# Kernel tuning notes

Measured on AMD Instinct MI355X. Metric: run time of the kernel, lower is better.

The kernel has to match this reference:

```python
import jax, jax.numpy as jnp
import numpy as np
import math

NUM_HEADS = 16


def setup_inputs() -> dict:
    key = jax.random.key(0)
    ks = jax.random.split(key, 5)
    L, B, E = 2048, 2, 1024
    scale = 1.0 / math.sqrt(E)
    return {
        "query": jax.random.normal(ks[0], (L, B, E), jnp.float32),
        "key": jax.random.normal(ks[1], (L, B, E), jnp.float32),
        "value": jax.random.normal(ks[2], (L, B, E), jnp.float32),
        "in_proj_weight": jax.random.normal(ks[3], (3 * E, E), jnp.float32) * scale,
        "in_proj_bias": jnp.zeros((3 * E,), jnp.float32),
        "out_w": jax.random.normal(ks[4], (E, E), jnp.float32) * scale,
        "out_b": jnp.zeros((E,), jnp.float32),
    }


def reference(query, key, value, in_proj_weight, in_proj_bias, out_w, out_b):
    L, Bz, E = query.shape
    S = key.shape[0]
    H = NUM_HEADS
    hd = E // H
    # in-projection: chunk packed weight into q/k/v parts (same math as torch chunk)
    w_q, w_k, w_v = jnp.split(in_proj_weight, 3, axis=0)
    b_q, b_k, b_v = jnp.split(in_proj_bias, 3, axis=0)
    q = query @ w_q.T + b_q            # (L, B, E)
    k = key @ w_k.T + b_k              # (S, B, E)
    v = value @ w_v.T + b_v            # (S, B, E)
    # (L, B*H, hd) -> (B*H, L, hd)
    q = q.reshape(L, Bz * H, hd).transpose(1, 0, 2) / math.sqrt(hd)
    k = k.reshape(S, Bz * H, hd).transpose(1, 0, 2)
    v = v.reshape(S, Bz * H, hd).transpose(1, 0, 2)
    # sigmoid attention (non-softmax), full (B*H, L, S) matrix as in original
    attn = jax.nn.sigmoid(jnp.einsum("bld,bsd->bls", q, k))
    denom = attn.sum(axis=-1, keepdims=True) + 1e-4
    out = jnp.einsum("bls,bsd->bld", attn / denom, v)  # (B*H, L, hd)
    out = out.transpose(1, 0, 2).reshape(L, Bz, E)
    out = out @ out_w.T + out_b
    avg_weights = attn.reshape(Bz, H, L, S).sum(axis=1) / H
    return out, avg_weights
```

## Files before the change

kernel.cpp:

```cpp
#include <hip/hip_runtime.h>
#include <stdint.h>


#define L_SEQ 2048
#define NBATCH 2
#define EMB 1024
#define NHEAD 16
#define HD 64
#define MROWS 4096

typedef __bf16 bf16x8 __attribute__((ext_vector_type(8)));
typedef float f32x4 __attribute__((ext_vector_type(4)));

#define WAITVM(N) asm volatile("s_waitcnt vmcnt(" #N ")" ::: "memory")
#define WAITLG() asm volatile("s_waitcnt lgkmcnt(0)" ::: "memory")
#define SBAR()                                  \
  do {                                          \
    asm volatile("" ::: "memory");              \
    __builtin_amdgcn_s_barrier();               \
    asm volatile("" ::: "memory");              \
  } while (0)

#if __has_builtin(__builtin_amdgcn_exp2f)
#define EXP2F(x) __builtin_amdgcn_exp2f(x)
#else
#define EXP2F(x) exp2f(x)
#endif

__device__ __forceinline__ unsigned short f2bf(float f) {
  union { float f; uint32_t u; } v; v.f = f;
  uint32_t u = v.u;
  u += 0x7fffu + ((u >> 16) & 1u);
  return (unsigned short)(u >> 16);
}

__device__ __forceinline__ unsigned short f2bf_fast(float f) {
  union { float f; uint32_t u; } v; v.f = f;
  return (unsigned short)((v.u + 0x8000u) >> 16);
}

__device__ __forceinline__ void gl_lds16(const void* gptr, void* ldsptr) {
  const uint32_t* g = reinterpret_cast<const uint32_t*>(gptr);
  auto* l = reinterpret_cast<__attribute__((address_space(3))) uint32_t*>(
      reinterpret_cast<uintptr_t>(ldsptr));
  __builtin_amdgcn_global_load_lds(g, l, 16, 0, 0);
}

__device__ __forceinline__ f32x4 mfma16(bf16x8 a, bf16x8 b, f32x4 c) {
  return __builtin_amdgcn_mfma_f32_16x16x32_bf16(a, b, c, 0, 0, 0);
}

__device__ __forceinline__ float fast_sigmoid2(float st) {
  float e = EXP2F(st);
  return __builtin_amdgcn_rcpf(1.0f + e);
}

__global__ __launch_bounds__(256) void k_convert(
    const float* __restrict__ qin, const float* __restrict__ kin,
    const float* __restrict__ vin, const float* __restrict__ win,
    const float* __restrict__ wo,
    unsigned short* __restrict__ Xq, unsigned short* __restrict__ Xk,
    unsigned short* __restrict__ Xv, unsigned short* __restrict__ Wb,
    unsigned short* __restrict__ Wob) {
  const int row = blockIdx.x;
  const int t = threadIdx.x;
  const float* src;
  unsigned short* dst;
  int srow;
  size_t drow;
  if (row < 3 * MROWS) {
    const int which = row >> 12;
    const int m = row & (MROWS - 1);
    const int b = m >> 11, l = m & (L_SEQ - 1);
    srow = l * NBATCH + b;
    drow = (size_t)m;
    src = which == 0 ? qin : (which == 1 ? kin : vin);
    dst = which == 0 ? Xq : (which == 1 ? Xk : Xv);
  } else if (row < 3 * MROWS + 3072) {
    srow = row - 3 * MROWS; drow = (size_t)srow; src = win; dst = Wb;
  } else {
    srow = row - (3 * MROWS + 3072); drow = (size_t)srow; src = wo; dst = Wob;
  }
  const float4 vv = *(const float4*)(src + (size_t)srow * EMB + t * 4);
  ushort4 o;
  o.x = f2bf(vv.x); o.y = f2bf(vv.y); o.z = f2bf(vv.z); o.w = f2bf(vv.w);
  *(ushort4*)(dst + drow * EMB + t * 4) = o;
}

__device__ __forceinline__ void gemm_issue(
    const unsigned short* __restrict__ A, const unsigned short* __restrict__ Bm,
    int m0, int n0, int k0, unsigned short* sA, unsigned short* sB) {
  const int tid = threadIdx.x;
  const int wave = tid >> 6;
  const int lane = tid & 63;
  const int srow = lane >> 2;
  const int scol = lane & 3;
  for (int i = 0; i < 2; ++i) {
    const int p = wave * 2 + i;
    const int r = p * 16 + srow;
    const int c = scol ^ ((r >> 1) & 3);
    gl_lds16(A + (size_t)(m0 + r) * EMB + k0 + c * 8, sA + p * 512);
    gl_lds16(Bm + (size_t)(n0 + r) * EMB + k0 + c * 8, sB + p * 512);
  }
}

__device__ __forceinline__ void gemm_core(
    const unsigned short* __restrict__ A, const unsigned short* __restrict__ Bm,
    int m0, int n0, unsigned short* sA, unsigned short* sB, f32x4 acc[4][4]) {
  const int tid = threadIdx.x;
  const int wave = tid >> 6;
  const int lane = tid & 63;
  const int quad = lane >> 4;
  const int l16 = lane & 15;
  const int wm = (wave >> 1) * 64;
  const int wn = (wave & 1) * 64;
  const int NSTEP = EMB / 32;

  for (int mi = 0; mi < 4; ++mi)
    for (int ni = 0; ni < 4; ++ni)
      acc[mi][ni] = (f32x4){0.f, 0.f, 0.f, 0.f};

  gemm_issue(A, Bm, m0, n0, 0, sA, sB);
  gemm_issue(A, Bm, m0, n0, 32, sA + 4096, sB + 4096);

  int cur = 0;
  for (int step = 0; step < NSTEP; ++step) {
    if (step < NSTEP - 1) { WAITVM(4); } else { WAITVM(0); }
    SBAR();
    if (step + 2 < NSTEP) {
      int nxt = cur + 2; if (nxt >= 3) nxt -= 3;
      gemm_issue(A, Bm, m0, n0, (step + 2) * 32, sA + nxt * 4096,
                 sB + nxt * 4096);
    }
    const unsigned short* cA = sA + cur * 4096;
    const unsigned short* cB = sB + cur * 4096;
    bf16x8 af[4], bfr[4];
    for (int mi = 0; mi < 4; ++mi) {
      const int r = wm + mi * 16 + l16;
      const int cp = quad ^ ((r >> 1) & 3);
      af[mi] = *(const bf16x8*)(cA + r * 32 + cp * 8);
    }
    for (int ni = 0; ni < 4; ++ni) {
      const int r = wn + ni * 16 + l16;
      const int cp = quad ^ ((r >> 1) & 3);
      bfr[ni] = *(const bf16x8*)(cB + r * 32 + cp * 8);
    }
    for (int mi = 0; mi < 4; ++mi)
      for (int ni = 0; ni < 4; ++ni)
        acc[mi][ni] = mfma16(af[mi], bfr[ni], acc[mi][ni]);
    cur = cur == 2 ? 0 : cur + 1;
  }
}

__global__ __launch_bounds__(256) void k_inproj(
    const unsigned short* __restrict__ Xq, const unsigned short* __restrict__ Xk,
    const unsigned short* __restrict__ Xv, const unsigned short* __restrict__ Wb,
    const float* __restrict__ bias,
    unsigned short* __restrict__ qb, unsigned short* __restrict__ kb,
    unsigned short* __restrict__ vb) {
  __shared__ __attribute__((aligned(16))) unsigned short sA[3 * 128 * 32];
  __shared__ __attribute__((aligned(16))) unsigned short sB[3 * 128 * 32];
  const int bid = blockIdx.x;
  const int tile = (bid & 7) * 96 + (bid >> 3);
  const int z = tile >> 8;
  const int rem = tile & 255;
  const int m0 = (rem >> 3) * 128;
  const int n0 = (rem & 7) * 128;
  const unsigned short* A = z == 0 ? Xq : (z == 1 ? Xk : Xv);
  f32x4 acc[4][4];
  gemm_core(A, Wb + (size_t)z * EMB * EMB, m0, n0, sA, sB, acc);

  const int tid = threadIdx.x, wave = tid >> 6, lane = tid & 63;
  const int quad = lane >> 4, l16 = lane & 15;
  const int wm = (wave >> 1) * 64, wn = (wave & 1) * 64;
  const float scale = (z == 0) ? -0.18033688011112042f : 1.0f;
  unsigned short* dst01 = (z == 0) ? qb : kb;
  for (int ni = 0; ni < 4; ++ni) {
    const int n = n0 + wn + ni * 16 + l16;
    const float bv = bias[z * EMB + n];
    const int h = n >> 6, d = n & 63;
    for (int mi = 0; mi < 4; ++mi) {
      for (int r = 0; r < 4; ++r) {
        const int m = m0 + wm + mi * 16 + quad * 4 + r;
        const int b = m >> 11, l = m & (L_SEQ - 1);
        const unsigned short o = f2bf((acc[mi][ni][r] + bv) * scale);
        if (z == 2)
          vb[((size_t)(b * NHEAD + h) * HD + d) * L_SEQ + l] = o;
        else
          dst01[((size_t)(b * NHEAD + h) * L_SEQ + l) * HD + d] = o;
      }
    }
  }
}

__global__ __launch_bounds__(512) void k_attn_avg(
    const unsigned short* __restrict__ qb, const unsigned short* __restrict__ kb,
    const unsigned short* __restrict__ vb, unsigned short* __restrict__ oh,
    float* __restrict__ avg) {
  __shared__ __attribute__((aligned(16))) unsigned short smem[32768];

  const int aid = blockIdx.x;
  const int tid = threadIdx.x, wave = tid >> 6, lane = tid & 63;
  const int quad = lane >> 4, l16 = lane & 15;
  const int sr8 = lane >> 3, sc8 = lane & 7;

  if (aid < 512) {
    unsigned short (*sK)[64 * 64] = (unsigned short (*)[64 * 64])(smem);
    unsigned short (*sV)[64 * 64] = (unsigned short (*)[64 * 64])(smem + 8192);
    unsigned short* sP = smem + 16384;

    const int bh = aid & 31;
    const int b = bh >> 4, h = bh & 15;
    const int l0 = (aid >> 5) * 128;
    const unsigned short* qg = qb + ((size_t)bh * L_SEQ + l0) * HD;
    const unsigned short* kg = kb + (size_t)bh * L_SEQ * HD;
    const unsigned short* vg = vb + (size_t)bh * HD * L_SEQ;

    const int W = wave * 16;

    bf16x8 qf0, qf1;
    {
      const unsigned short* qrow = qg + (size_t)(W + l16) * HD + quad * 8;
      qf0 = *(const bf16x8*)(qrow);
      qf1 = *(const bf16x8*)(qrow + 32);
    }

    if (wave < 4) {
      for (int i = 0; i < 2; ++i) {
        const int p = wave * 2 + i;
        const int r = p * 8 + sr8;
        const int c = sc8 ^ (r & 7);
        gl_lds16(kg + (size_t)r * HD + c * 8, sK[0] + p * 512);
      }
    } else {
      for (int i = 0; i < 2; ++i) {
        const int p = (wave - 4) * 2 + i;
        const int r = p * 8 + sr8;
        const int c = sc8 ^ (r & 7);
        gl_lds16(vg + (size_t)r * L_SEQ + c * 8, sV[0] + p * 512);
      }
    }

    f32x4 oacc[4];
    for (int ni = 0; ni < 4; ++ni) oacc[ni] = (f32x4){0.f, 0.f, 0.f, 0.f};
    f32x4 dacc = (f32x4){0.f, 0.f, 0.f, 0.f};

    bf16x8 ones;
    for (int j = 0; j < 8; ++j) ones[j] = (__bf16)1.0f;

    const int NS = L_SEQ / 64;
    for (int it = 0; it < NS; ++it) {
      const int cur = it & 1;
      WAITVM(0);
      SBAR();
      if (it + 1 < NS) {
        const int s0n = (it + 1) * 64;
        if (wave < 4) {
          for (int i = 0; i < 2; ++i) {
            const int p = wave * 2 + i;
            const int r = p * 8 + sr8;
            const int c = sc8 ^ (r & 7);
            gl_lds16(kg + (size_t)(s0n + r) * HD + c * 8, sK[cur ^ 1] + p * 512);
          }
        } else {
          for (int i = 0; i < 2; ++i) {
            const int p = (wave - 4) * 2 + i;
            const int r = p * 8 + sr8;
            const int c = sc8 ^ (r & 7);
            gl_lds16(vg + (size_t)r * L_SEQ + s0n + c * 8, sV[cur ^ 1] + p * 512);
          }
        }
      }

      f32x4 st[4];
      for (int smi = 0; smi < 4; ++smi) st[smi] = (f32x4){0.f, 0.f, 0.f, 0.f};
      {
        for (int smi = 0; smi < 4; ++smi) {
          const int r = smi * 16 + l16;
          const int c = quad ^ (r & 7);
          bf16x8 a = *(const bf16x8*)(sK[cur] + r * 64 + c * 8);
          st[smi] = mfma16(a, qf0, st[smi]);
        }
      }
      {
        for (int smi = 0; smi < 4; ++smi) {
          const int r = smi * 16 + l16;
          const int c = (4 + quad) ^ (r & 7);
          bf16x8 a = *(const bf16x8*)(sK[cur] + r * 64 + c * 8);
          st[smi] = mfma16(a, qf1, st[smi]);
        }
      }

      for (int smi = 0; smi < 4; ++smi) {
        uint32_t u[4];
        for (int r = 0; r < 4; ++r) {
          union { float f; uint32_t i; } cv;
          cv.f = fast_sigmoid2(st[smi][r]);
          u[r] = cv.i + 0x8000u;
        }
        uint2 pk;
        pk.x = __builtin_amdgcn_perm(u[1], u[0], 0x07060302u);
        pk.y = __builtin_amdgcn_perm(u[3], u[2], 0x07060302u);
        *(uint2*)(sP + (size_t)(W + l16) * 72 + smi * 16 + quad * 4) = pk;
      }
      WAITLG();

      const int lr = W + l16;
      for (int kk = 0; kk < 64; kk += 32) {
        bf16x8 ap = *(const bf16x8*)(sP + (size_t)lr * 72 + kk + quad * 8);
        for (int ni = 0; ni < 4; ++ni) {
          const int rd = ni * 16 + l16;
          const int c = ((kk >> 3) + quad) ^ (rd & 7);
          bf16x8 bv4 = *(const bf16x8*)(sV[cur] + rd * 64 + c * 8);
          oacc[ni] = mfma16(ap, bv4, oacc[ni]);
        }
        dacc = mfma16(ap, ones, dacc);
      }
    }

    for (int r = 0; r < 4; ++r) {
      const int lrow = l0 + wave * 16 + quad * 4 + r;
      const float rden = __builtin_amdgcn_rcpf(dacc[r] + 1e-4f);
      unsigned short* dst = oh + ((size_t)(b * L_SEQ + lrow)) * EMB + h * HD;
      for (int ni = 0; ni < 4; ++ni)
        dst[ni * 16 + l16] = f2bf_fast(oacc[ni][r] * rden);
    }
  } else {
    unsigned short (*sQ)[128 * 64] = (unsigned short (*)[128 * 64])(smem);
    unsigned short (*sK)[128 * 64] = (unsigned short (*)[128 * 64])(smem + 16384);

    const int avgid = aid - 512;
    const int ss0 = (avgid & 15) * 128;
    const int l0 = ((avgid >> 4) & 15) * 128;
    const int b = avgid >> 8;
    const int wm = (wave & 1) * 64, wn = (wave >> 1) * 32;

    f32x4 av[4][2];
    for (int mi = 0; mi < 4; ++mi)
      for (int ni = 0; ni < 2; ++ni) av[mi][ni] = (f32x4){0.f, 0.f, 0.f, 0.f};

    auto stage = [&](int hh, int buf) {
      const unsigned short* qg =
          qb + ((size_t)(b * NHEAD + hh) * L_SEQ + l0) * HD;
      const unsigned short* kg =
          kb + ((size_t)(b * NHEAD + hh) * L_SEQ + ss0) * HD;
      for (int i = 0; i < 2; ++i) {
        const int p = wave * 2 + i;
        const int r = p * 8 + sr8;
        const int c = sc8 ^ (r & 7);
        gl_lds16(qg + (size_t)r * HD + c * 8, sQ[buf] + p * 512);
        gl_lds16(kg + (size_t)r * HD + c * 8, sK[buf] + p * 512);
      }
    };

    stage(0, 0);

    for (int h = 0; h < NHEAD; ++h) {
      const int cur = h & 1;
      WAITVM(0);
      SBAR();
      if (h + 1 < NHEAD) stage(h + 1, cur ^ 1);

      f32x4 scr[4][2];
      for (int mi = 0; mi < 4; ++mi)
        for (int ni = 0; ni < 2; ++ni) scr[mi][ni] = (f32x4){0.f, 0.f, 0.f, 0.f};
      for (int kk = 0; kk < HD; kk += 32) {
        bf16x8 a[4], bbv[2];
        for (int mi = 0; mi < 4; ++mi) {
          const int r = wm + mi * 16 + l16;
          const int c = ((kk >> 3) + quad) ^ (r & 7);
          a[mi] = *(const bf16x8*)(sQ[cur] + r * 64 + c * 8);
        }
        for (int ni = 0; ni < 2; ++ni) {
          const int r = wn + ni * 16 + l16;
          const int c = ((kk >> 3) + quad) ^ (r & 7);
          bbv[ni] = *(const bf16x8*)(sK[cur] + r * 64 + c * 8);
        }
        for (int mi = 0; mi < 4; ++mi)
          for (int ni = 0; ni < 2; ++ni)
            scr[mi][ni] = mfma16(a[mi], bbv[ni], scr[mi][ni]);
      }
      for (int mi = 0; mi < 4; ++mi)
        for (int ni = 0; ni < 2; ++ni)
          for (int r = 0; r < 4; ++r)
            av[mi][ni][r] += fast_sigmoid2(scr[mi][ni][r]);
    }

    for (int mi = 0; mi < 4; ++mi) {
      for (int r = 0; r < 4; ++r) {
        const int l = l0 + wm + mi * 16 + quad * 4 + r;
        float* dst = avg + ((size_t)b * L_SEQ + l) * L_SEQ + ss0 + wn;
        for (int ni = 0; ni < 2; ++ni)
          dst[ni * 16 + l16] = av[mi][ni][r] * 0.0625f;
      }
    }
  }
}

__global__ __launch_bounds__(256) void k_outproj(
    const unsigned short* __restrict__ OH, const unsigned short* __restrict__ Wob,
    const float* __restrict__ ob, float* __restrict__ out) {
  __shared__ __attribute__((aligned(16))) unsigned short sA[3 * 128 * 32];
  __shared__ __attribute__((aligned(16))) unsigned short sB[3 * 128 * 32];
  const int bid = blockIdx.x;
  const int tile = (bid & 7) * 32 + (bid >> 3);
  const int m0 = (tile >> 3) * 128;
  const int n0 = (tile & 7) * 128;
  f32x4 acc[4][4];
  gemm_core(OH, Wob, m0, n0, sA, sB, acc);

  const int tid = threadIdx.x, wave = tid >> 6, lane = tid & 63;
  const int quad = lane >> 4, l16 = lane & 15;
  const int wm = (wave >> 1) * 64, wn = (wave & 1) * 64;
  for (int ni = 0; ni < 4; ++ni) {
    const int n = n0 + wn + ni * 16 + l16;
    const float bv = ob[n];
    for (int mi = 0; mi < 4; ++mi) {
      for (int r = 0; r < 4; ++r) {
        const int m = m0 + wm + mi * 16 + quad * 4 + r;
        const int b = m >> 11, l = m & (L_SEQ - 1);
        out[((size_t)l * NBATCH + b) * EMB + n] = acc[mi][ni][r] + bv;
      }
    }
  }
}

extern "C" void kernel_launch(void* const* d_in, const int* in_sizes, int n_in,
                              void* d_out, int out_size, void* d_ws, size_t ws_size,
                              hipStream_t stream) {
  (void)in_sizes; (void)n_in; (void)out_size;
  const float* qin = (const float*)d_in[0];
  const float* kin = (const float*)d_in[1];
  const float* vin = (const float*)d_in[2];
  const float* w   = (const float*)d_in[3];
  const float* bias = (const float*)d_in[4];
  const float* wo  = (const float*)d_in[5];
  const float* ob  = (const float*)d_in[6];
  float* out = (float*)d_out;

  unsigned short* Xq  = (unsigned short*)d_ws;
  unsigned short* Xk  = Xq + (size_t)MROWS * EMB;
  unsigned short* Xv  = Xk + (size_t)MROWS * EMB;
  unsigned short* Wb  = Xv + (size_t)MROWS * EMB;
  unsigned short* Wob = Wb + (size_t)3 * EMB * EMB;
  unsigned short* qbuf = Wob + (size_t)EMB * EMB;
  unsigned short* kbuf = qbuf + (size_t)MROWS * EMB;
  unsigned short* vbuf = kbuf + (size_t)MROWS * EMB;
  unsigned short* ohb  = vbuf + (size_t)MROWS * EMB;
  const size_t need = ((size_t)MROWS * EMB * 7 + (size_t)4 * EMB * EMB) * 2;
  if (ws_size < need) return;

  k_convert<<<16384, 256, 0, stream>>>(qin, kin, vin, w, wo, Xq, Xk, Xv, Wb, Wob);
  k_inproj<<<768, 256, 0, stream>>>(Xq, Xk, Xv, Wb, bias, qbuf, kbuf, vbuf);
  k_attn_avg<<<1024, 512, 0, stream>>>(qbuf, kbuf, vbuf, ohb,
                                       out + (size_t)MROWS * EMB);
  k_outproj<<<256, 256, 0, stream>>>(ohb, Wob, ob, out);
}
```

Measured before the change: 256.7 us.

## Double query rows per attention block to reuse K/V tiles across two groups

Each attention block now handles 256 query rows instead of 128, with each wave processing two 16-row groups that share every K and V fragment loaded from LDS. This halves the number of attention blocks and the K/V global/LDS traffic per query row. The sP region grows to hold 256 rows, enlarging shared memory, and launch bounds now request a minimum of 4 waves per SIMD. The larger per-wave register footprint and fewer blocks may reduce occupancy or load balance against the avg-weight blocks.

Measured after the change: 250.9 us. 2.3% less time.

```diff
diff --git a/kernel.cpp b/kernel.cpp
--- a/kernel.cpp
+++ b/kernel.cpp
@@ -193,36 +193,37 @@
   }
 }
 
-__global__ __launch_bounds__(512) void k_attn_avg(
+__global__ __launch_bounds__(512, 4) void k_attn_avg(
     const unsigned short* __restrict__ qb, const unsigned short* __restrict__ kb,
     const unsigned short* __restrict__ vb, unsigned short* __restrict__ oh,
     float* __restrict__ avg) {
-  __shared__ __attribute__((aligned(16))) unsigned short smem[32768];
+  __shared__ __attribute__((aligned(16))) unsigned short smem[34816];
 
   const int aid = blockIdx.x;
   const int tid = threadIdx.x, wave = tid >> 6, lane = tid & 63;
   const int quad = lane >> 4, l16 = lane & 15;
   const int sr8 = lane >> 3, sc8 = lane & 7;
 
-  if (aid < 512) {
+  if (aid < 256) {
     unsigned short (*sK)[64 * 64] = (unsigned short (*)[64 * 64])(smem);
     unsigned short (*sV)[64 * 64] = (unsigned short (*)[64 * 64])(smem + 8192);
     unsigned short* sP = smem + 16384;
 
     const int bh = aid & 31;
     const int b = bh >> 4, h = bh & 15;
-    const int l0 = (aid >> 5) * 128;
+    const int l0 = (aid >> 5) * 256;
     const unsigned short* qg = qb + ((size_t)bh * L_SEQ + l0) * HD;
     const unsigned short* kg = kb + (size_t)bh * L_SEQ * HD;
     const unsigned short* vg = vb + (size_t)bh * HD * L_SEQ;
 
-    const int W = wave * 16;
-
-    bf16x8 qf0, qf1;
-    {
-      const unsigned short* qrow = qg + (size_t)(W + l16) * HD + quad * 8;
-      qf0 = *(const bf16x8*)(qrow);
-      qf1 = *(const bf16x8*)(qrow + 32);
+    const int W = wave * 32;
+
+    bf16x8 qf[2][2];
+    for (int g = 0; g < 2; ++g) {
+      const unsigned short* qrow =
+          qg + (size_t)(W + g * 16 + l16) * HD + quad * 8;
+      qf[g][0] = *(const bf16x8*)(qrow);
+      qf[g][1] = *(const bf16x8*)(qrow + 32);
     }
 
     if (wave < 4) {
@@ -241,9 +242,12 @@
       }
     }
 
-    f32x4 oacc[4];
-    for (int ni = 0; ni < 4; ++ni) oacc[ni] = (f32x4){0.f, 0.f, 0.f, 0.f};
-    f32x4 dacc = (f32x4){0.f, 0.f, 0.f, 0.f};
+    f32x4 oacc[2][4];
+    f32x4 dacc[2];
+    for (int g = 0; g < 2; ++g) {
+      for (int ni = 0; ni < 4; ++ni) oacc[g][ni] = (f32x4){0.f, 0.f, 0.f, 0.f};
+      dacc[g] = (f32x4){0.f, 0.f, 0.f, 0.f};
+    }
 
     bf16x8 ones;
     for (int j = 0; j < 8; ++j) ones[j] = (__bf16)1.0f;
@@ -272,14 +276,16 @@
         }
       }
 
-      f32x4 st[4];
-      for (int smi = 0; smi < 4; ++smi) st[smi] = (f32x4){0.f, 0.f, 0.f, 0.f};
+      f32x4 st[2][4];
+      for (int g = 0; g < 2; ++g)
+        for (int smi = 0; smi < 4; ++smi) st[g][smi] = (f32x4){0.f, 0.f, 0.f, 0.f};
       {
         for (int smi = 0; smi < 4; ++smi) {
           const int r = smi * 16 + l16;
           const int c = quad ^ (r & 7);
           bf16x8 a = *(const bf16x8*)(sK[cur] + r * 64 + c * 8);
-          st[smi] = mfma16(a, qf0, st[smi]);
+          st[0][smi] = mfma16(a, qf[0][0], st[0][smi]);
+          st[1][smi] = mfma16(a, qf[1][0], st[1][smi]);
         }
       }
       {
@@ -287,49 +293,73 @@
           const int r = smi * 16 + l16;
           const int c = (4 + quad) ^ (r & 7);
           bf16x8 a = *(const bf16x8*)(sK[cur] + r * 64 + c * 8);
-          st[smi] = mfma16(a, qf1, st[smi]);
-        }
-      }
-
-      for (int smi = 0; smi < 4; ++smi) {
-        uint32_t u[4];
-        for (int r = 0; r < 4; ++r) {
-          union { float f; uint32_t i; } cv;
-          cv.f = fast_sigmoid2(st[smi][r]);
-          u[r] = cv.i + 0x8000u;
-        }
-        uint2 pk;
-        pk.x = __builtin_amdgcn_perm(u[1], u[0], 0x07060302u);
-        pk.y = __builtin_amdgcn_perm(u[3], u[2], 0x07060302u);
-        *(uint2*)(sP + (size_t)(W + l16) * 72 + smi * 16 + quad * 4) = pk;
+          st[0][smi] = mfma16(a, qf[0][1], st[0][smi]);
+          st[1][smi] = mfma16(a, qf[1][1], st[1][smi]);
+        }
+      }
+
+      for (int g = 0; g < 2; ++g) {
+        for (int smi = 0; smi < 4; ++smi) {
+          uint32_t u[4];
+          for (int r = 0; r < 4; ++r) {
+            union { float f; uint32_t i; } cv;
+            cv.f = fast_sigmoid2(st[g][smi][r]);
+            u[r] = cv.i + 0x8000u;
+          }
+          uint2 pk;
+          pk.x = __builtin_amdgcn_perm(u[1], u[0], 0x07060302u);
+          pk.y = __builtin_amdgcn_perm(u[3], u[2], 0x07060302u);
+          *(uint2*)(sP + (size_t)(W + g * 16 + l16) * 72 + smi * 16 + quad * 4) =
+              pk;
+        }
       }
       WAITLG();
 
-      const int lr = W + l16;
-      for (int kk = 0; kk < 64; kk += 32) {
-        bf16x8 ap = *(const bf16x8*)(sP + (size_t)lr * 72 + kk + quad * 8);
+      {
+        bf16x8 ap0 = *(const bf16x8*)(sP + (size_t)(W + l16) * 72 + quad * 8);
+        bf16x8 ap1 =
+            *(const bf16x8*)(sP + (size_t)(W + 16 + l16) * 72 + quad * 8);
         for (int ni = 0; ni < 4; ++ni) {
           const int rd = ni * 16 + l16;
-          const int c = ((kk >> 3) + quad) ^ (rd & 7);
+          const int c = quad ^ (rd & 7);
           bf16x8 bv4 = *(const bf16x8*)(sV[cur] + rd * 64 + c * 8);
-          oacc[ni] = mfma16(ap, bv4, oacc[ni]);
-        }
-        dacc = mfma16(ap, ones, dacc);
-      }
-    }
-
-    for (int r = 0; r < 4; ++r) {
-      const int lrow = l0 + wave * 16 + quad * 4 + r;
-      const float rden = __builtin_amdgcn_rcpf(dacc[r] + 1e-4f);
-      unsigned short* dst = oh + ((size_t)(b * L_SEQ + lrow)) * EMB + h * HD;
-      for (int ni = 0; ni < 4; ++ni)
-        dst[ni * 16 + l16] = f2bf_fast(oacc[ni][r] * rden);
+          oacc[0][ni] = mfma16(ap0, bv4, oacc[0][ni]);
+          oacc[1][ni] = mfma16(ap1, bv4, oacc[1][ni]);
+        }
+        dacc[0] = mfma16(ap0, ones, dacc[0]);
+        dacc[1] = mfma16(ap1, ones, dacc[1]);
+      }
+      {
+        bf16x8 ap0 =
+            *(const bf16x8*)(sP + (size_t)(W + l16) * 72 + 32 + quad * 8);
+        bf16x8 ap1 =
+            *(const bf16x8*)(sP + (size_t)(W + 16 + l16) * 72 + 32 + quad * 8);
+        for (int ni = 0; ni < 4; ++ni) {
+          const int rd = ni * 16 + l16;
+          const int c = (4 + quad) ^ (rd & 7);
+          bf16x8 bv4 = *(const bf16x8*)(sV[cur] + rd * 64 + c * 8);
+          oacc[0][ni] = mfma16(ap0, bv4, oacc[0][ni]);
+          oacc[1][ni] = mfma16(ap1, bv4, oacc[1][ni]);
+        }
+        dacc[0] = mfma16(ap0, ones, dacc[0]);
+        dacc[1] = mfma16(ap1, ones, dacc[1]);
+      }
+    }
+
+    for (int g = 0; g < 2; ++g) {
+      for (int r = 0; r < 4; ++r) {
+        const int lrow = l0 + W + g * 16 + quad * 4 + r;
+        const float rden = __builtin_amdgcn_rcpf(dacc[g][r] + 1e-4f);
+        unsigned short* dst = oh + ((size_t)(b * L_SEQ + lrow)) * EMB + h * HD;
+        for (int ni = 0; ni < 4; ++ni)
+          dst[ni * 16 + l16] = f2bf_fast(oacc[g][ni][r] * rden);
+      }
     }
   } else {
     unsigned short (*sQ)[128 * 64] = (unsigned short (*)[128 * 64])(smem);
     unsigned short (*sK)[128 * 64] = (unsigned short (*)[128 * 64])(smem + 16384);
 
-    const int avgid = aid - 512;
+    const int avgid = aid - 256;
     const int ss0 = (avgid & 15) * 128;
     const int l0 = ((avgid >> 4) & 15) * 128;
     const int b = avgid >> 8;
@@ -452,7 +482,7 @@
 
   k_convert<<<16384, 256, 0, stream>>>(qin, kin, vin, w, wo, Xq, Xk, Xv, Wb, Wob);
   k_inproj<<<768, 256, 0, stream>>>(Xq, Xk, Xv, Wb, bias, qbuf, kbuf, vbuf);
-  k_attn_avg<<<1024, 512, 0, stream>>>(qbuf, kbuf, vbuf, ohb,
-                                       out + (size_t)MROWS * EMB);
+  k_attn_avg<<<768, 512, 0, stream>>>(qbuf, kbuf, vbuf, ohb,
+                                      out + (size_t)MROWS * EMB);
   k_outproj<<<256, 256, 0, stream>>>(ohb, Wob, ob, out);
 }
```
